# Optimization experiments

Hardware: AMD Instinct MI355X
Metric: run time of the kernel (lower is better)

The kernel has to match this reference:

```python
import jax, jax.numpy as jnp
import numpy as np

N_NODES = 100000
N_EDGES = 1600000
D_IN = 128
D_EMB = 128


def setup_inputs() -> dict:
    key = jax.random.key(0)
    ks = jax.random.split(key, 8)
    x = jax.random.normal(ks[0], (N_NODES, D_IN), dtype=jnp.float32)
    src = jax.random.randint(ks[1], (N_EDGES,), 0, N_NODES, dtype=jnp.int32)
    dst = jax.random.randint(ks[2], (N_EDGES,), 0, N_NODES, dtype=jnp.int32)
    # Glorot-ish init for GraphConv weights
    s = 1.0 / np.sqrt(D_EMB)
    W0 = jax.random.normal(ks[3], (D_IN, D_EMB), dtype=jnp.float32) * s
    W1 = jax.random.normal(ks[4], (D_EMB, D_EMB), dtype=jnp.float32) * s
    W2 = jax.random.normal(ks[5], (D_EMB, D_EMB), dtype=jnp.float32) * s
    b0 = jnp.zeros((D_EMB,), jnp.float32)
    b1 = jnp.zeros((D_EMB,), jnp.float32)
    b2 = jnp.zeros((D_EMB,), jnp.float32)
    return {"x": x, "src": src, "dst": dst,
            "W0": W0, "b0": b0, "W1": W1, "b1": b1, "W2": W2, "b2": b2}


def _graph_conv(h, src, dst, norm_src, norm_dst, W, b):
    # DGL GraphConv, norm='both': D_out^{-1/2} A D_in^{-1/2} H W + b
    h = h * norm_src[:, None]                       # scale src features
    m = jax.ops.segment_sum(h[src], dst, num_segments=N_NODES)  # SpMM aggregate
    m = m * norm_dst[:, None]
    return m @ W + b


def reference(x, src, dst, W0, b0, W1, b1, W2, b2):
    ones = jnp.ones((N_EDGES,), jnp.float32)
    out_deg = jax.ops.segment_sum(ones, src, num_segments=N_NODES)
    in_deg = jax.ops.segment_sum(ones, dst, num_segments=N_NODES)
    norm_src = jax.lax.rsqrt(jnp.clip(out_deg, 1.0))
    norm_dst = jax.lax.rsqrt(jnp.clip(in_deg, 1.0))

    h = x
    Ws = (W0, W1, W2)
    bs = (b0, b1, b2)
    n_layers = len(Ws)
    for layer in range(n_layers):
        h = _graph_conv(h, src, dst, norm_src, norm_dst, Ws[layer], bs[layer])
        if layer != n_layers - 1:
            h = jax.nn.relu(h)  # dropout is identity in eval mode
    return h
```

## Files before the change

### kernel.cpp

```cpp
#include <hip/hip_runtime.h>
#include <hip/hip_bf16.h>

#define N_NODES 100000
#define N_EDGES 1600000
#define D 128
#define NB 1563
#define PB 256
#define CHUNK 6250
#define SCANL (NB * PB)
#define SGRID (SCANL / 256)
#define SENT N_NODES
#define ECAP_PAD (N_EDGES + 256 * NB)

typedef __attribute__((ext_vector_type(8))) short bf16x8;
typedef __attribute__((ext_vector_type(4))) float f32x4;

__device__ __forceinline__ float bf2f(unsigned short u) {
    unsigned int x = ((unsigned int)u) << 16;
    return __builtin_bit_cast(float, x);
}
__device__ __forceinline__ unsigned short f2bf(float f) {
    unsigned int x = __builtin_bit_cast(unsigned int, f);
    x += 0x7fffu + ((x >> 16) & 1u);
    return (unsigned short)(x >> 16);
}
__device__ __forceinline__ void accum8(float* acc, uint4 x) {
    acc[0] += bf2f((unsigned short)x.x); acc[1] += bf2f((unsigned short)(x.x >> 16));
    acc[2] += bf2f((unsigned short)x.y); acc[3] += bf2f((unsigned short)(x.y >> 16));
    acc[4] += bf2f((unsigned short)x.z); acc[5] += bf2f((unsigned short)(x.z >> 16));
    acc[6] += bf2f((unsigned short)x.w); acc[7] += bf2f((unsigned short)(x.w >> 16));
}

__global__ __launch_bounds__(1024) void k_pcount(const int* __restrict__ src, const int* __restrict__ dst,
                                                 int* __restrict__ cntD, int* __restrict__ cntS) {
    __shared__ int hd[NB];
    __shared__ int hs[NB];
    int t = threadIdx.x, blk = blockIdx.x;
    for (int i = t; i < NB; i += 1024) { hd[i] = 0; hs[i] = 0; }
    __syncthreads();
    int base = blk * CHUNK;
    for (int i = t; i < CHUNK; i += 1024) {
        int e = base + i;
        atomicAdd(&hd[dst[e] >> 6], 1);
        atomicAdd(&hs[src[e] >> 6], 1);
    }
    __syncthreads();
    for (int i = t; i < NB; i += 1024) {
        cntD[i * PB + blk] = hd[i];
        cntS[i * PB + blk] = hs[i];
    }
}

__global__ void k_scanDS1(int* __restrict__ cntD, int* __restrict__ cntS, int* __restrict__ bs) {
    __shared__ int tmp[256];
    int t = threadIdx.x;
    int which = (blockIdx.x >= SGRID) ? 1 : 0;
    int blk = blockIdx.x - which * SGRID;
    int* a = which ? cntS : cntD;
    int i = blk * 256 + t;
    int v = a[i];
    tmp[t] = v; __syncthreads();
    for (int off = 1; off < 256; off <<= 1) {
        int x = (t >= off) ? tmp[t - off] : 0;
        __syncthreads();
        tmp[t] += x;
        __syncthreads();
    }
    a[i] = tmp[t] - v;
    if (t == 255) bs[blockIdx.x] = tmp[255];
}

__global__ void k_scan2two(int* __restrict__ bs) {
    __shared__ int tmp[1024];
    int t = threadIdx.x;
    int base = blockIdx.x * SGRID;
    int i0 = 2 * t, i1 = 2 * t + 1;
    int a = (i0 < SGRID) ? bs[base + i0] : 0;
    int b = (i1 < SGRID) ? bs[base + i1] : 0;
    int s = a + b;
    tmp[t] = s; __syncthreads();
    for (int off = 1; off < 1024; off <<= 1) {
        int x = (t >= off) ? tmp[t - off] : 0;
        __syncthreads();
        tmp[t] += x;
        __syncthreads();
    }
    int excl = tmp[t] - s;
    if (i0 < SGRID) bs[base + i0] = excl;
    if (i1 < SGRID) bs[base + i1] = excl + a;
}

__global__ void k_scanDS3(int* __restrict__ cntD, int* __restrict__ cntS, const int* __restrict__ bs) {
    int which = (blockIdx.x >= SGRID) ? 1 : 0;
    int blk = blockIdx.x - which * SGRID;
    int* a = which ? cntS : cntD;
    a[blk * 256 + threadIdx.x] += bs[blockIdx.x];
}

__global__ __launch_bounds__(1024) void k_pscatter(const int* __restrict__ src, const int* __restrict__ dst,
                                                   const int* __restrict__ scanD, const int* __restrict__ scanS,
                                                   unsigned int* __restrict__ pairD, unsigned char* __restrict__ srcS) {
    __shared__ int od[NB];
    __shared__ int osx[NB];
    int t = threadIdx.x, blk = blockIdx.x;
    for (int i = t; i < NB; i += 1024) {
        od[i] = scanD[i * PB + blk];
        osx[i] = scanS[i * PB + blk];
    }
    __syncthreads();
    int base = blk * CHUNK;
    for (int i = t; i < CHUNK; i += 1024) {
        int e = base + i;
        int s = src[e], d = dst[e];
        int pd = atomicAdd(&od[d >> 6], 1);
        pairD[pd] = ((unsigned int)(d & 63) << 26) | (unsigned int)s;
        int ps = atomicAdd(&osx[s >> 6], 1);
        srcS[ps] = (unsigned char)(s & 63);
    }
}

__global__ __launch_bounds__(256) void k_normsrc(const unsigned char* __restrict__ srcS,
                                                 const int* __restrict__ scanS, float* __restrict__ ns) {
    __shared__ int c[64];
    int b = blockIdx.x, t = threadIdx.x;
    if (t < 64) c[t] = 0;
    __syncthreads();
    int beg = scanS[b * PB];
    int end = (b < NB - 1) ? scanS[(b + 1) * PB] : N_EDGES;
    for (int i = beg + t; i < end; i += 256) atomicAdd(&c[srcS[i]], 1);
    __syncthreads();
    if (t < 64) {
        int g = b * 64 + t;
        if (g < N_NODES) {
            int a = c[t]; if (a < 1) a = 1;
            ns[g] = rsqrtf((float)a);
        }
    }
}

__global__ __launch_bounds__(256) void k_bsortpad(const unsigned int* __restrict__ pairD,
                                                  const int* __restrict__ scanD,
                                                  int* __restrict__ esrc,
                                                  int* __restrict__ rowbeg,
                                                  int* __restrict__ degD) {
    __shared__ int cnt[64], off[64], cur[64];
    int b = blockIdx.x, t = threadIdx.x;
    int lane = t & 63, wave = t >> 6;
    if (t < 64) cnt[t] = 0;
    __syncthreads();
    int beg = scanD[b * PB];
    int end = (b < NB - 1) ? scanD[(b + 1) * PB] : N_EDGES;
    int n = end - beg;
    int base = beg + 256 * b;
    for (int i = t; i < n; i += 256) atomicAdd(&cnt[pairD[beg + i] >> 26], 1);
    __syncthreads();
    if (wave == 0) {
        int v = cnt[lane];
        int pc = (v + 3) & ~3;
        int x = pc;
        for (int o = 1; o < 64; o <<= 1) { int y = __shfl_up(x, o); if (lane >= o) x += y; }
        off[lane] = x - pc;
        cur[lane] = x - pc;
    }
    __syncthreads();
    if (t < 64) {
        int g = b * 64 + t;
        if (g < N_NODES) { rowbeg[g] = base + off[t]; degD[g] = cnt[t]; }
    }
    {
        int r = t >> 2, j = t & 3;
        int c0 = cnt[r];
        int slot = off[r] + c0 + j;
        if (slot < off[r] + ((c0 + 3) & ~3)) esrc[base + slot] = SENT;
    }
    for (int i = t; i < n; i += 256) {
        unsigned int p = pairD[beg + i];
        int pos = atomicAdd(&cur[p >> 26], 1);
        esrc[base + pos] = (int)(p & 0x3FFFFFFu);
    }
}

__global__ void k_cvt(const float* __restrict__ x, const float* __restrict__ ns,
                      unsigned short* __restrict__ hA, unsigned short* __restrict__ hB, int n4) {
    int i = blockIdx.x * 256 + threadIdx.x;
    if (i < n4) {
        int row = i >> 5;
        float sc = ns[row];
        const float4 v = ((const float4*)x)[i];
        unsigned int lo = (unsigned int)f2bf(v.x * sc) | ((unsigned int)f2bf(v.y * sc) << 16);
        unsigned int hi = (unsigned int)f2bf(v.z * sc) | ((unsigned int)f2bf(v.w * sc) << 16);
        ((uint2*)hA)[i] = make_uint2(lo, hi);
    } else if (i < n4 + 64) {
        int j = i - n4;
        uint2 z = {0u, 0u};
        if (j < 32) ((uint2*)(hA + (size_t)SENT * D))[j] = z;
        else        ((uint2*)(hB + (size_t)SENT * D))[j - 32] = z;
    }
}

__global__ void k_transw3(const float* __restrict__ W0, const float* __restrict__ W1,
                          const float* __restrict__ W2, unsigned short* __restrict__ Wt) {
    int gid = blockIdx.x * 256 + threadIdx.x;
    if (gid >= 3 * 2048) return;
    int layer = gid >> 11;
    int di8   = gid & 2047;
    const float* W = (layer == 0) ? W0 : ((layer == 1) ? W1 : W2);
    int di   = di8 * 8;
    int lane = di8 & 63;
    int nt   = (di8 >> 6) & 7;
    int kc   = di8 >> 9;
    int quad = lane >> 4, col = lane & 15;
    unsigned short v[8];
#pragma unroll
    for (int j = 0; j < 8; j++) {
        int k = kc * 32 + quad * 8 + j;
        int nn = nt * 16 + col;
        v[j] = f2bf(W[k * 128 + nn]);
    }
    unsigned short* dp = Wt + (size_t)layer * 16384 + di;
#pragma unroll
    for (int j = 0; j < 8; j++) dp[j] = v[j];
}

__device__ __forceinline__ int aswz(int row, int byte16) {
    return row * 256 + (byte16 ^ ((row & 7) << 4));
}

__global__ __launch_bounds__(256, 8) void k_fused(const unsigned short* __restrict__ hin,
        const int* __restrict__ esrc, const int* __restrict__ rowbeg, const int* __restrict__ degD,
        const float* __restrict__ nsp,
        const unsigned short* __restrict__ Wt, const float* __restrict__ bias,
        unsigned short* __restrict__ Cb, float* __restrict__ Cf, int M) {
    __shared__ int rb[64];
    __shared__ int dgt[64];
    __shared__ unsigned short lA[64 * 128];
    int b = blockIdx.x, t = threadIdx.x;
    int lane = t & 63, wave = t >> 6;
    int sub = lane >> 4, col = lane & 15;

    if (t < 64) {
        int g = b * 64 + t;
        rb[t]  = (g < M) ? rowbeg[g] : 0;
        dgt[t] = (g < M) ? degD[g] : 0;
    }
    __syncthreads();

    for (int r = wave; r < 64; r += 4) {
        int ro = rb[r];
        int dgr = dgt[r];
        int re = ro + ((dgr + 3) & ~3);
        float acc[8];
#pragma unroll
        for (int j = 0; j < 8; j++) acc[j] = 0.f;
        int e = ro;
        for (; e + 16 <= re; e += 16) {
            int s0 = esrc[e + sub];
            int s1 = esrc[e + 4 + sub];
            int s2 = esrc[e + 8 + sub];
            int s3 = esrc[e + 12 + sub];
            uint4 x0 = *(const uint4*)(hin + (size_t)s0 * D + col * 8);
            uint4 x1 = *(const uint4*)(hin + (size_t)s1 * D + col * 8);
            uint4 x2 = *(const uint4*)(hin + (size_t)s2 * D + col * 8);
            uint4 x3 = *(const uint4*)(hin + (size_t)s3 * D + col * 8);
            accum8(acc, x0); accum8(acc, x1); accum8(acc, x2); accum8(acc, x3);
        }
        for (; e < re; e += 4) {
            int s = esrc[e + sub];
            uint4 x = *(const uint4*)(hin + (size_t)s * D + col * 8);
            accum8(acc, x);
        }
#pragma unroll
        for (int j = 0; j < 8; j++) {
            acc[j] += __shfl_xor(acc[j], 16);
            acc[j] += __shfl_xor(acc[j], 32);
        }
        if (sub == 0) {
            int d2 = dgr; if (d2 < 1) d2 = 1;
            float s = rsqrtf((float)d2);
            uint4 o;
            o.x = (unsigned int)f2bf(acc[0] * s) | ((unsigned int)f2bf(acc[1] * s) << 16);
            o.y = (unsigned int)f2bf(acc[2] * s) | ((unsigned int)f2bf(acc[3] * s) << 16);
            o.z = (unsigned int)f2bf(acc[4] * s) | ((unsigned int)f2bf(acc[5] * s) << 16);
            o.w = (unsigned int)f2bf(acc[6] * s) | ((unsigned int)f2bf(acc[7] * s) << 16);
            *(uint4*)((char*)lA + aswz(r, col * 16)) = o;
        }
    }
    __syncthreads();

    int row0 = b * 64 + wave * 16;
    float nsv[4];
    if (Cb) {
#pragma unroll
        for (int r = 0; r < 4; r++) {
            int rr = row0 + sub * 4 + r;
            nsv[r] = (rr < M) ? nsp[rr] : 1.f;
        }
    }
#pragma unroll
    for (int half = 0; half < 2; half++) {
        f32x4 acc2[4];
#pragma unroll
        for (int i = 0; i < 4; i++) acc2[i] = (f32x4){0.f, 0.f, 0.f, 0.f};
        int lr = wave * 16 + col;
#pragma unroll
        for (int kc = 0; kc < 4; kc++) {
            bf16x8 af = *(const bf16x8*)((const char*)lA + aswz(lr, kc * 64 + sub * 16));
#pragma unroll
            for (int j = 0; j < 4; j++) {
                int nt = half * 4 + j;
                bf16x8 bfr = *(const bf16x8*)(Wt + ((size_t)(kc * 8 + nt) * 64 + lane) * 8);
                acc2[j] = __builtin_amdgcn_mfma_f32_16x16x32_bf16(af, bfr, acc2[j], 0, 0, 0);
            }
        }
#pragma unroll
        for (int j = 0; j < 4; j++) {
            int nt = half * 4 + j;
            float bv = bias[nt * 16 + col];
#pragma unroll
            for (int r = 0; r < 4; r++) {
                int rr = row0 + sub * 4 + r;
                if (rr < M) {
                    float v = acc2[j][r] + bv;
                    if (Cf) {
                        Cf[(size_t)rr * D + nt * 16 + col] = v;
                    } else {
                        v = fmaxf(v, 0.f) * nsv[r];
                        Cb[(size_t)rr * D + nt * 16 + col] = f2bf(v);
                    }
                }
            }
        }
    }
}

extern "C" void kernel_launch(void* const* d_in, const int* in_sizes, int n_in,
                              void* d_out, int out_size, void* d_ws, size_t ws_size,
                              hipStream_t stream) {
    const float* x  = (const float*)d_in[0];
    const int* src = (const int*)d_in[1];
    const int* dst = (const int*)d_in[2];
    const float* Wl[3] = {(const float*)d_in[3], (const float*)d_in[5], (const float*)d_in[7]};
    const float* Bl[3] = {(const float*)d_in[4], (const float*)d_in[6], (const float*)d_in[8]};

    const int N = N_NODES;
    const int Mpad = ((N + 63) / 64) * 64;

    char* ws = (char*)d_ws;
    size_t o = 0;
    auto take = [&](size_t bytes) -> void* {
        o = (o + 255) & ~(size_t)255;
        void* p = ws + o;
        o += bytes;
        return p;
    };
    int*   cntD     = (int*)take((size_t)SCANL * 4);
    int*   cntS     = (int*)take((size_t)SCANL * 4);
    int*   bs       = (int*)take((size_t)2 * SGRID * 4);
    float* norm_src = (float*)take((size_t)N * 4);
    unsigned int*  pairD = (unsigned int*)take((size_t)N_EDGES * 4);
    unsigned char* srcS  = (unsigned char*)take((size_t)N_EDGES);
    int*   esrc     = (int*)take((size_t)ECAP_PAD * 4);
    int*   rowbeg   = (int*)take((size_t)N * 4);
    int*   degD     = (int*)take((size_t)N * 4);
    unsigned short* Wt   = (unsigned short*)take((size_t)3 * 128 * 128 * 2);
    unsigned short* hA   = (unsigned short*)take((size_t)Mpad * D * 2);
    unsigned short* hB   = (unsigned short*)take((size_t)Mpad * D * 2);

    k_pcount<<<PB, 1024, 0, stream>>>(src, dst, cntD, cntS);
    k_scanDS1<<<2 * SGRID, 256, 0, stream>>>(cntD, cntS, bs);
    k_scan2two<<<2, 1024, 0, stream>>>(bs);
    k_scanDS3<<<2 * SGRID, 256, 0, stream>>>(cntD, cntS, bs);
    k_pscatter<<<PB, 1024, 0, stream>>>(src, dst, cntD, cntS, pairD, srcS);
    k_normsrc<<<NB, 256, 0, stream>>>(srcS, cntS, norm_src);
    k_bsortpad<<<NB, 256, 0, stream>>>(pairD, cntD, esrc, rowbeg, degD);

    k_cvt<<<(N * 32 + 64 + 255) / 256, 256, 0, stream>>>(x, norm_src, hA, hB, N * 32);
    k_transw3<<<24, 256, 0, stream>>>(Wl[0], Wl[1], Wl[2], Wt);

    k_fused<<<NB, 256, 0, stream>>>(hA, esrc, rowbeg, degD, norm_src, Wt,         Bl[0], hB, nullptr, N);
    k_fused<<<NB, 256, 0, stream>>>(hB, esrc, rowbeg, degD, norm_src, Wt + 16384, Bl[1], hA, nullptr, N);
    k_fused<<<NB, 256, 0, stream>>>(hA, esrc, rowbeg, degD, norm_src, Wt + 32768, Bl[2], nullptr, (float*)d_out, N);
}
```

Before: 408.4 us.

## Double partition blocks, permute count columns, stage sorted edges in LDS, alias workspace

Raises the edge-partition block count from 256 to 512 with smaller chunks, and permutes the column index used to store per-block counts. Each scan thread now handles two elements to cover the larger count array. The bucket sort writes its sorted, sentinel-padded edge list into a shared-memory staging buffer first, then copies it to global memory contiguously, replacing scattered global writes. The preprocessing buffers are overlaid on the hB feature buffer, which shrinks the workspace footprint. The risk is that a bucket whose padded size exceeds the fixed 2816-entry staging capacity would be silently truncated.

```diff
diff --git a/kernel.cpp b/kernel.cpp
--- a/kernel.cpp
+++ b/kernel.cpp
@@ -5,12 +5,13 @@
 #define N_EDGES 1600000
 #define D 128
 #define NB 1563
-#define PB 256
-#define CHUNK 6250
+#define PB 512
+#define CHUNK 3125
 #define SCANL (NB * PB)
-#define SGRID (SCANL / 256)
+#define SGRID (SCANL / 512)
 #define SENT N_NODES
 #define ECAP_PAD (N_EDGES + 256 * NB)
+#define BCAP 2816
 
 typedef __attribute__((ext_vector_type(8))) short bf16x8;
 typedef __attribute__((ext_vector_type(4))) float f32x4;
@@ -30,12 +31,14 @@
     acc[4] += bf2f((unsigned short)x.z); acc[5] += bf2f((unsigned short)(x.z >> 16));
     acc[6] += bf2f((unsigned short)x.w); acc[7] += bf2f((unsigned short)(x.w >> 16));
 }
+__device__ __forceinline__ int XP(int b) { return ((b & 7) << 6) | (b >> 3); }
 
 __global__ __launch_bounds__(1024) void k_pcount(const int* __restrict__ src, const int* __restrict__ dst,
                                                  int* __restrict__ cntD, int* __restrict__ cntS) {
     __shared__ int hd[NB];
     __shared__ int hs[NB];
     int t = threadIdx.x, blk = blockIdx.x;
+    int col = XP(blk);
     for (int i = t; i < NB; i += 1024) { hd[i] = 0; hs[i] = 0; }
     __syncthreads();
     int base = blk * CHUNK;
@@ -46,8 +49,8 @@
     }
     __syncthreads();
     for (int i = t; i < NB; i += 1024) {
-        cntD[i * PB + blk] = hd[i];
-        cntS[i * PB + blk] = hs[i];
+        cntD[i * PB + col] = hd[i];
+        cntS[i * PB + col] = hs[i];
     }
 }
 
@@ -57,16 +60,19 @@
     int which = (blockIdx.x >= SGRID) ? 1 : 0;
     int blk = blockIdx.x - which * SGRID;
     int* a = which ? cntS : cntD;
-    int i = blk * 256 + t;
-    int v = a[i];
-    tmp[t] = v; __syncthreads();
+    int base = blk * 512;
+    int a0 = a[base + 2 * t], a1 = a[base + 2 * t + 1];
+    int s = a0 + a1;
+    tmp[t] = s; __syncthreads();
     for (int off = 1; off < 256; off <<= 1) {
         int x = (t >= off) ? tmp[t - off] : 0;
         __syncthreads();
         tmp[t] += x;
         __syncthreads();
     }
-    a[i] = tmp[t] - v;
+    int excl = tmp[t] - s;
+    a[base + 2 * t] = excl;
+    a[base + 2 * t + 1] = excl + a0;
     if (t == 255) bs[blockIdx.x] = tmp[255];
 }
 
@@ -94,7 +100,11 @@
     int which = (blockIdx.x >= SGRID) ? 1 : 0;
     int blk = blockIdx.x - which * SGRID;
     int* a = which ? cntS : cntD;
-    a[blk * 256 + threadIdx.x] += bs[blockIdx.x];
+    int v = bs[blockIdx.x];
+    int base = blk * 512;
+    int t = threadIdx.x;
+    a[base + 2 * t] += v;
+    a[base + 2 * t + 1] += v;
 }
 
 __global__ __launch_bounds__(1024) void k_pscatter(const int* __restrict__ src, const int* __restrict__ dst,
@@ -103,9 +113,10 @@
     __shared__ int od[NB];
     __shared__ int osx[NB];
     int t = threadIdx.x, blk = blockIdx.x;
+    int col = XP(blk);
     for (int i = t; i < NB; i += 1024) {
-        od[i] = scanD[i * PB + blk];
-        osx[i] = scanS[i * PB + blk];
+        od[i] = scanD[i * PB + col];
+        osx[i] = scanS[i * PB + col];
     }
     __syncthreads();
     int base = blk * CHUNK;
@@ -144,6 +155,8 @@
                                                   int* __restrict__ rowbeg,
                                                   int* __restrict__ degD) {
     __shared__ int cnt[64], off[64], cur[64];
+    __shared__ int ptotS;
+    __shared__ int stage[BCAP];
     int b = blockIdx.x, t = threadIdx.x;
     int lane = t & 63, wave = t >> 6;
     if (t < 64) cnt[t] = 0;
@@ -161,23 +174,23 @@
         for (int o = 1; o < 64; o <<= 1) { int y = __shfl_up(x, o); if (lane >= o) x += y; }
         off[lane] = x - pc;
         cur[lane] = x - pc;
-    }
-    __syncthreads();
+        if (lane == 63) ptotS = x;
+    }
+    __syncthreads();
+    int ptot = ptotS; if (ptot > BCAP) ptot = BCAP;
     if (t < 64) {
         int g = b * 64 + t;
         if (g < N_NODES) { rowbeg[g] = base + off[t]; degD[g] = cnt[t]; }
     }
-    {
-        int r = t >> 2, j = t & 3;
-        int c0 = cnt[r];
-        int slot = off[r] + c0 + j;
-        if (slot < off[r] + ((c0 + 3) & ~3)) esrc[base + slot] = SENT;
-    }
+    for (int i = t; i < ptot; i += 256) stage[i] = SENT;
+    __syncthreads();
     for (int i = t; i < n; i += 256) {
         unsigned int p = pairD[beg + i];
         int pos = atomicAdd(&cur[p >> 26], 1);
-        esrc[base + pos] = (int)(p & 0x3FFFFFFu);
-    }
+        if (pos < BCAP) stage[pos] = (int)(p & 0x3FFFFFFu);
+    }
+    __syncthreads();
+    for (int i = t; i < ptot; i += 256) esrc[base + i] = stage[i];
 }
 
 __global__ void k_cvt(const float* __restrict__ x, const float* __restrict__ ns,
@@ -344,27 +357,30 @@
 
     const int N = N_NODES;
     const int Mpad = ((N + 63) / 64) * 64;
+    const size_t HBYTES = (size_t)Mpad * D * 2;
 
     char* ws = (char*)d_ws;
-    size_t o = 0;
+
+    unsigned short* hB = (unsigned short*)ws;
+    int* cntD = (int*)ws;
+    int* cntS = (int*)(ws + (size_t)SCANL * 4);
+    unsigned int*  pairD = (unsigned int*)(ws + (size_t)2 * SCANL * 4);
+    unsigned char* srcS  = (unsigned char*)(ws + (size_t)2 * SCANL * 4 + (size_t)N_EDGES * 4);
+    int* bs = (int*)(ws + (size_t)2 * SCANL * 4 + (size_t)N_EDGES * 5);
+
+    size_t o = HBYTES;
     auto take = [&](size_t bytes) -> void* {
         o = (o + 255) & ~(size_t)255;
         void* p = ws + o;
         o += bytes;
         return p;
     };
-    int*   cntD     = (int*)take((size_t)SCANL * 4);
-    int*   cntS     = (int*)take((size_t)SCANL * 4);
-    int*   bs       = (int*)take((size_t)2 * SGRID * 4);
     float* norm_src = (float*)take((size_t)N * 4);
-    unsigned int*  pairD = (unsigned int*)take((size_t)N_EDGES * 4);
-    unsigned char* srcS  = (unsigned char*)take((size_t)N_EDGES);
     int*   esrc     = (int*)take((size_t)ECAP_PAD * 4);
     int*   rowbeg   = (int*)take((size_t)N * 4);
     int*   degD     = (int*)take((size_t)N * 4);
-    unsigned short* Wt   = (unsigned short*)take((size_t)3 * 128 * 128 * 2);
-    unsigned short* hA   = (unsigned short*)take((size_t)Mpad * D * 2);
-    unsigned short* hB   = (unsigned short*)take((size_t)Mpad * D * 2);
+    unsigned short* Wt = (unsigned short*)take((size_t)3 * 128 * 128 * 2);
+    unsigned short* hA = (unsigned short*)take(HBYTES);
 
     k_pcount<<<PB, 1024, 0, stream>>>(src, dst, cntD, cntS);
     k_scanDS1<<<2 * SGRID, 256, 0, stream>>>(cntD, cntS, bs);
```

Result: faster. 387.7 us (-5.1%).
